# Kernel optimization log

Hardware: AMD Instinct MI355X
Metric: run time of the kernel (lower is better)

The kernel has to match this reference:

```python
import jax, jax.numpy as jnp
import numpy as np

B, S, D, E, H, K = 2, 2048, 1024, 8, 4096, 2


def setup_inputs() -> dict:
    key = jax.random.key(0)
    ks = jax.random.split(key, 8)
    w = lambda i, shape: jax.random.normal(ks[i], shape, jnp.float32) * 0.02
    return {
        "x": jax.random.normal(ks[0], (B, S, D), jnp.float32),
        "noise": jax.random.normal(ks[1], (B, S, E), jnp.float32),
        "Wg": w(2, (E, D)),
        "noise_weight": jnp.zeros((E,), jnp.float32),
        "W1": w(3, (E, D, H)),
        "b1": jnp.zeros((E, H), jnp.float32),
        "W2": w(4, (E, D, H)),
        "b2": jnp.zeros((E, H), jnp.float32),
        "Wp": w(5, (E, H, D)),
        "bp": jnp.zeros((E, D), jnp.float32),
        "k": K,
    }


def reference(x, noise, Wg, noise_weight, W1, b1, W2, b2, Wp, bp, k):
    Bb, Ss, Dd = x.shape
    Ee = Wg.shape[0]
    # --- noisy top-k gate (noisy_std = 1.0) ---
    logits = jnp.einsum('bsd,ed->bse', x, Wg)
    noisy = logits + noise * noise_weight            # [B,S,E]
    vals, idx = jax.lax.top_k(noisy, k)              # [B,S,k]
    oh = jax.nn.one_hot(idx, Ee, dtype=x.dtype)      # [B,S,k,E]
    sel = oh.sum(axis=-2) > 0                        # [B,S,E] selected mask
    scat = (oh * vals[..., None]).sum(axis=-2)       # scatter topk logits
    sparse = jnp.where(sel, scat, -jnp.inf)
    gate = jax.nn.softmax(sparse, axis=-1)           # zero weight off-topk
    # --- dense-equivalent expert compute (gate==0 off top-k => same math as masked dispatch) ---
    xf = x.reshape(Bb * Ss, Dd)                      # [T,D]
    gf = gate.reshape(Bb * Ss, Ee)                   # [T,E]
    h1 = jnp.einsum('td,edh->eth', xf, W1) + b1[:, None, :]
    h2 = jnp.einsum('td,edh->eth', xf, W2) + b2[:, None, :]
    hh = h1 * jax.nn.silu(h2)                        # SwiGLU
    outs = jnp.einsum('eth,ehd->etd', hh, Wp) + bp[:, None, :]
    final = jnp.einsum('etd,te->td', outs, gf).reshape(Bb, Ss, Dd)
    return final, idx
```

## Files before the change

kernel.cpp:

```cpp
#include <hip/hip_runtime.h>
#include <math.h>

#define Bc 2
#define Sc 2048
#define Dc 1024
#define Ec 8
#define Hc 4096
#define Tc (Bc*Sc)
#define NSLOT (Tc*2)
#define FINAL_N ((size_t)Tc*Dc)
#define BK 32

typedef float f32x4 __attribute__((ext_vector_type(4)));
typedef __bf16 bf16x8 __attribute__((ext_vector_type(8)));

__device__ __forceinline__ unsigned short f2bf(float f) {
    union { float f; unsigned int u; } v; v.f = f;
    return (unsigned short)((v.u + 0x7fffu + ((v.u >> 16) & 1u)) >> 16);
}

__device__ __forceinline__ void gload16(const unsigned short* g, unsigned short* l) {
    __builtin_amdgcn_global_load_lds(
        (const __attribute__((address_space(1))) unsigned int*)g,
        (__attribute__((address_space(3))) unsigned int*)l,
        16, 0, 0);
}

__global__ void k_cvt_x(const float* __restrict__ x, unsigned short* __restrict__ xbf) {
    int gid = blockIdx.x * 256 + threadIdx.x;
    const float4* p = (const float4*)x + (size_t)gid * 2;
    float4 a = p[0], b = p[1];
    ushort4 r0 = { f2bf(a.x), f2bf(a.y), f2bf(a.z), f2bf(a.w) };
    ushort4 r1 = { f2bf(b.x), f2bf(b.y), f2bf(b.z), f2bf(b.w) };
    ushort4* o = (ushort4*)xbf + (size_t)gid * 2;
    o[0] = r0; o[1] = r1;
}

__global__ void k_transpose_cvt2(const float* __restrict__ inA, const float* __restrict__ inB,
                                 unsigned short* __restrict__ outA, unsigned short* __restrict__ outB,
                                 int R, int C, int nz_per_mat) {
    __shared__ float tile[64][65];
    int z = blockIdx.z;
    const float* in; unsigned short* out;
    if (z < nz_per_mat) { in = inA; out = outA; }
    else { in = inB; out = outB; z -= nz_per_mat; }
    size_t base = (size_t)z * (size_t)R * C;
    int cb = blockIdx.x * 64, rb = blockIdx.y * 64;
    int t = threadIdx.x;
    int q = t & 15, g = t >> 4;
    #pragma unroll
    for (int j = 0; j < 4; j++) {
        int row = g + 16*j;
        float4 v = *(const float4*)&in[base + (size_t)(rb+row)*C + cb + q*4];
        tile[row][q*4+0] = v.x; tile[row][q*4+1] = v.y;
        tile[row][q*4+2] = v.z; tile[row][q*4+3] = v.w;
    }
    __syncthreads();
    #pragma unroll
    for (int j = 0; j < 4; j++) {
        int co = g + 16*j;
        ushort4 o;
        o.x = f2bf(tile[q*4+0][co]); o.y = f2bf(tile[q*4+1][co]);
        o.z = f2bf(tile[q*4+2][co]); o.w = f2bf(tile[q*4+3][co]);
        *(ushort4*)&out[base + (size_t)(cb+co)*R + rb + q*4] = o;
    }
}

__global__ void k_gate(const float* __restrict__ x, const float* __restrict__ noise,
                       const float* __restrict__ Wg, const float* __restrict__ nw,
                       float* __restrict__ out_idx, int* __restrict__ counts,
                       int* __restrict__ tok_top, float* __restrict__ tok_w) {
    int t = blockIdx.x;
    int lane = threadIdx.x;
    const float* xr = x + (size_t)t * Dc;
    double acc[Ec];
    #pragma unroll
    for (int e = 0; e < Ec; e++) acc[e] = 0.0;
    for (int i = 0; i < Dc/64; i++) {
        int d = lane + i*64;
        double xv = (double)xr[d];
        #pragma unroll
        for (int e = 0; e < Ec; e++) acc[e] += xv * (double)Wg[e*Dc + d];
    }
    #pragma unroll
    for (int e = 0; e < Ec; e++)
        for (int off = 32; off > 0; off >>= 1)
            acc[e] += __shfl_down(acc[e], off);
    if (lane == 0) {
        double noisy[Ec];
        #pragma unroll
        for (int e = 0; e < Ec; e++)
            noisy[e] = acc[e] + (double)noise[t*Ec + e] * (double)nw[e];
        int i0 = 0;
        for (int e = 1; e < Ec; e++) if (noisy[e] > noisy[i0]) i0 = e;
        int i1 = -1;
        for (int e = 0; e < Ec; e++) {
            if (e == i0) continue;
            if (i1 < 0 || noisy[e] > noisy[i1]) i1 = e;
        }
        double ee = exp(noisy[i1] - noisy[i0]);
        float w0 = (float)(1.0 / (1.0 + ee));
        float w1 = (float)(ee / (1.0 + ee));
        out_idx[t*2 + 0] = (float)i0;
        out_idx[t*2 + 1] = (float)i1;
        tok_top[t*2] = i0; tok_top[t*2+1] = i1;
        tok_w[t*2] = w0;   tok_w[t*2+1] = w1;
        atomicAdd(&counts[i0], 1);
        atomicAdd(&counts[i1], 1);
    }
}

__global__ void k_scan(const int* __restrict__ counts, int* __restrict__ offsets) {
    if (threadIdx.x == 0) {
        int s = 0;
        for (int e = 0; e < Ec; e++) { offsets[e] = s; s += counts[e]; }
        offsets[Ec] = s;
    }
}

__global__ void k_fill(const int* __restrict__ tok_top, const int* __restrict__ offsets,
                       int* __restrict__ fill, int* __restrict__ slot_token,
                       int* __restrict__ slot_of) {
    int t = blockIdx.x * 256 + threadIdx.x;
    if (t >= Tc) return;
    #pragma unroll
    for (int j = 0; j < 2; j++) {
        int e = tok_top[t*2 + j];
        int pos = atomicAdd(&fill[e], 1);
        int slot = offsets[e] + pos;
        slot_token[slot] = t;
        slot_of[t*2 + j] = slot;
    }
}

__global__ __launch_bounds__(256, 2) void k_gemm1(
    const unsigned short* __restrict__ xbf,
    const unsigned short* __restrict__ w1t, const unsigned short* __restrict__ w2t,
    const float* __restrict__ b1, const float* __restrict__ b2,
    const int* __restrict__ counts, const int* __restrict__ offsets,
    const int* __restrict__ slot_token,
    unsigned short* __restrict__ hh) {
    int e = blockIdx.z;
    int n_e = counts[e];
    int m0 = blockIdx.y * 128;
    if (m0 >= n_e) return;
    int base = offsets[e];
    int n0 = blockIdx.x * 128;

    __shared__ __align__(16) unsigned short lA0[128*BK],  lB10[128*BK], lB20[128*BK];
    __shared__ __align__(16) unsigned short lA1[128*BK],  lB11[128*BK], lB21[128*BK];
    __shared__ int tlist[128];

    int tid = threadIdx.x;
    if (tid < 128) {
        int r = m0 + tid; if (r > n_e - 1) r = n_e - 1;
        tlist[tid] = slot_token[base + r];
    }
    __syncthreads();

    int wid = tid >> 6, lane = tid & 63;
    int wr = wid >> 1, wc = wid & 1;

    int rl = lane >> 2, s = lane & 3;
    int r0 = wid*32 + rl, r1 = r0 + 16;
    int c0 = s ^ ((r0 >> 1) & 3);
    int c1 = s ^ ((r1 >> 1) & 3);
    int t0 = tlist[r0], t1 = tlist[r1];
    const size_t wbase = ((size_t)e * Hc + n0) * Dc;
    const unsigned short* pa0  = xbf + (size_t)t0*Dc + c0*8;
    const unsigned short* pa1  = xbf + (size_t)t1*Dc + c1*8;
    const unsigned short* pb10 = w1t + wbase + (size_t)r0*Dc + c0*8;
    const unsigned short* pb11 = w1t + wbase + (size_t)r1*Dc + c1*8;
    const unsigned short* pb20 = w2t + wbase + (size_t)r0*Dc + c0*8;
    const unsigned short* pb21 = w2t + wbase + (size_t)r1*Dc + c1*8;
    int wofs = wid*1024;

    f32x4 acc1[4][4], acc2[4][4];
    #pragma unroll
    for (int m = 0; m < 4; m++)
        #pragma unroll
        for (int n = 0; n < 4; n++)
            #pragma unroll
            for (int j = 0; j < 4; j++) { acc1[m][n][j] = 0.0f; acc2[m][n][j] = 0.0f; }

    int arow = lane & 15, cr = lane >> 4;

    auto STAGE = [&](unsigned short* dA, unsigned short* dB1, unsigned short* dB2, int kk) {
        gload16(pa0  + kk, dA  + wofs);  gload16(pa1  + kk, dA  + wofs + 512);
        gload16(pb10 + kk, dB1 + wofs);  gload16(pb11 + kk, dB1 + wofs + 512);
        gload16(pb20 + kk, dB2 + wofs);  gload16(pb21 + kk, dB2 + wofs + 512);
    };
    auto COMPUTE = [&](const unsigned short* lA, const unsigned short* lB1,
                       const unsigned short* lB2) {
        bf16x8 a[4], bb1[4], bb2[4];
        #pragma unroll
        for (int m = 0; m < 4; m++) {
            int rr = wr*64 + m*16 + arow;
            int cc = cr ^ ((rr >> 1) & 3);
            a[m] = *(const bf16x8*)&lA[rr*BK + cc*8];
        }
        #pragma unroll
        for (int n = 0; n < 4; n++) {
            int rr = wc*64 + n*16 + arow;
            int cc = cr ^ ((rr >> 1) & 3);
            bb1[n] = *(const bf16x8*)&lB1[rr*BK + cc*8];
            bb2[n] = *(const bf16x8*)&lB2[rr*BK + cc*8];
        }
        #pragma unroll
        for (int m = 0; m < 4; m++)
            #pragma unroll
            for (int n = 0; n < 4; n++) {
                acc1[m][n] = __builtin_amdgcn_mfma_f32_16x16x32_bf16(a[m], bb1[n], acc1[m][n], 0, 0, 0);
                acc2[m][n] = __builtin_amdgcn_mfma_f32_16x16x32_bf16(a[m], bb2[n], acc2[m][n], 0, 0, 0);
            }
    };

    STAGE(lA0, lB10, lB20, 0);
    __syncthreads();
    const int NT = Dc / BK;
    for (int t = 0; t < NT; t += 2) {
        STAGE(lA1, lB11, lB21, (t+1)*BK);
        COMPUTE(lA0, lB10, lB20);
        __syncthreads();
        if (t + 2 < NT) STAGE(lA0, lB10, lB20, (t+2)*BK);
        COMPUTE(lA1, lB11, lB21);
        __syncthreads();
    }

    int lrow = (lane >> 4) * 4, lcol = lane & 15;
    #pragma unroll
    for (int n = 0; n < 4; n++) {
        int hcol = n0 + wc*64 + n*16 + lcol;
        float bias1 = b1[e*Hc + hcol], bias2 = b2[e*Hc + hcol];
        #pragma unroll
        for (int m = 0; m < 4; m++) {
            int rb = m0 + wr*64 + m*16 + lrow;
            #pragma unroll
            for (int j = 0; j < 4; j++) {
                int r = rb + j;
                if (r < n_e) {
                    float h1v = acc1[m][n][j] + bias1;
                    float h2v = acc2[m][n][j] + bias2;
                    float hhv = h1v * (h2v / (1.0f + expf(-h2v)));
                    hh[(size_t)(base + r)*Hc + hcol] = f2bf(hhv);
                }
            }
        }
    }
}

__global__ __launch_bounds__(256, 2) void k_gemm2(
    const unsigned short* __restrict__ hh,
    const unsigned short* __restrict__ wpt,
    const float* __restrict__ bp,
    const int* __restrict__ counts, const int* __restrict__ offsets,
    float* __restrict__ outb) {
    int e = blockIdx.z;
    int n_e = counts[e];
    int m0 = blockIdx.y * 128;
    if (m0 >= n_e) return;
    int base = offsets[e];
    int n0 = blockIdx.x * 128;

    __shared__ __align__(16) unsigned short lA0[128*BK], lB0[128*BK];
    __shared__ __align__(16) unsigned short lA1[128*BK], lB1[128*BK];

    int tid = threadIdx.x;
    int wid = tid >> 6, lane = tid & 63;
    int wr = wid >> 1, wc = wid & 1;

    int rl = lane >> 2, s = lane & 3;
    int r0 = wid*32 + rl, r1 = r0 + 16;
    int c0 = s ^ ((r0 >> 1) & 3);
    int c1 = s ^ ((r1 >> 1) & 3);
    int ar0 = m0 + r0; if (ar0 > n_e - 1) ar0 = n_e - 1;
    int ar1 = m0 + r1; if (ar1 > n_e - 1) ar1 = n_e - 1;
    const size_t wb = ((size_t)e * Dc + n0) * Hc;
    const unsigned short* pa0 = hh  + (size_t)(base + ar0)*Hc + c0*8;
    const unsigned short* pa1 = hh  + (size_t)(base + ar1)*Hc + c1*8;
    const unsigned short* pb0 = wpt + wb + (size_t)r0*Hc + c0*8;
    const unsigned short* pb1 = wpt + wb + (size_t)r1*Hc + c1*8;
    int wofs = wid*1024;

    f32x4 acc[4][4];
    #pragma unroll
    for (int m = 0; m < 4; m++)
        #pragma unroll
        for (int n = 0; n < 4; n++)
            #pragma unroll
            for (int j = 0; j < 4; j++) acc[m][n][j] = 0.0f;

    int arow = lane & 15, cr = lane >> 4;

    auto STAGE = [&](unsigned short* dA, unsigned short* dB, int kk) {
        gload16(pa0 + kk, dA + wofs);  gload16(pa1 + kk, dA + wofs + 512);
        gload16(pb0 + kk, dB + wofs);  gload16(pb1 + kk, dB + wofs + 512);
    };
    auto COMPUTE = [&](const unsigned short* lA, const unsigned short* lB) {
        bf16x8 a[4], b[4];
        #pragma unroll
        for (int m = 0; m < 4; m++) {
            int rr = wr*64 + m*16 + arow;
            int cc = cr ^ ((rr >> 1) & 3);
            a[m] = *(const bf16x8*)&lA[rr*BK + cc*8];
        }
        #pragma unroll
        for (int n = 0; n < 4; n++) {
            int rr = wc*64 + n*16 + arow;
            int cc = cr ^ ((rr >> 1) & 3);
            b[n] = *(const bf16x8*)&lB[rr*BK + cc*8];
        }
        #pragma unroll
        for (int m = 0; m < 4; m++)
            #pragma unroll
            for (int n = 0; n < 4; n++)
                acc[m][n] = __builtin_amdgcn_mfma_f32_16x16x32_bf16(a[m], b[n], acc[m][n], 0, 0, 0);
    };

    STAGE(lA0, lB0, 0);
    __syncthreads();
    const int NT = Hc / BK;
    for (int t = 0; t < NT; t += 2) {
        STAGE(lA1, lB1, (t+1)*BK);
        COMPUTE(lA0, lB0);
        __syncthreads();
        if (t + 2 < NT) STAGE(lA0, lB0, (t+2)*BK);
        COMPUTE(lA1, lB1);
        __syncthreads();
    }

    int lrow = (lane >> 4) * 4, lcol = lane & 15;
    #pragma unroll
    for (int n = 0; n < 4; n++) {
        int dcol = n0 + wc*64 + n*16 + lcol;
        float bias = bp[e*Dc + dcol];
        #pragma unroll
        for (int m = 0; m < 4; m++) {
            int rb = m0 + wr*64 + m*16 + lrow;
            #pragma unroll
            for (int j = 0; j < 4; j++) {
                int r = rb + j;
                if (r < n_e)
                    outb[(size_t)(base + r)*Dc + dcol] = acc[m][n][j] + bias;
            }
        }
    }
}

__global__ void k_combine(const float* __restrict__ outb, const int* __restrict__ slot_of,
                          const float* __restrict__ tok_w, float* __restrict__ final_out) {
    int gid = blockIdx.x * 256 + threadIdx.x;
    int t = gid >> 8;
    int c = (gid & 255) * 4;
    int s0 = slot_of[t*2], s1 = slot_of[t*2 + 1];
    float w0 = tok_w[t*2], w1 = tok_w[t*2 + 1];
    float4 o0 = *(const float4*)&outb[(size_t)s0*Dc + c];
    float4 o1 = *(const float4*)&outb[(size_t)s1*Dc + c];
    float4 r;
    r.x = w0*o0.x + w1*o1.x;
    r.y = w0*o0.y + w1*o1.y;
    r.z = w0*o0.z + w1*o1.z;
    r.w = w0*o0.w + w1*o1.w;
    *(float4*)&final_out[(size_t)t*Dc + c] = r;
}

extern "C" void kernel_launch(void* const* d_in, const int* in_sizes, int n_in,
                              void* d_out, int out_size, void* d_ws, size_t ws_size,
                              hipStream_t stream) {
    (void)in_sizes; (void)n_in; (void)out_size; (void)ws_size;
    const float* x     = (const float*)d_in[0];
    const float* noise = (const float*)d_in[1];
    const float* Wg    = (const float*)d_in[2];
    const float* nw    = (const float*)d_in[3];
    const float* W1    = (const float*)d_in[4];
    const float* b1    = (const float*)d_in[5];
    const float* W2    = (const float*)d_in[6];
    const float* b2    = (const float*)d_in[7];
    const float* Wp    = (const float*)d_in[8];
    const float* bp    = (const float*)d_in[9];

    char* ws = (char*)d_ws;
    size_t off = 0;
    unsigned short* XBF = (unsigned short*)(ws + off); off += (size_t)Tc*Dc*2;
    unsigned short* W1T = (unsigned short*)(ws + off); off += (size_t)Ec*Dc*Hc*2;
    unsigned short* W2T = (unsigned short*)(ws + off); off += (size_t)Ec*Dc*Hc*2;
    unsigned short* WPT = (unsigned short*)(ws + off); off += (size_t)Ec*Hc*Dc*2;
    unsigned short* HH  = (unsigned short*)(ws + off); off += (size_t)NSLOT*Hc*2;
    float*          OUTB= (float*)(ws + off);          off += (size_t)NSLOT*Dc*4;
    int*   counts    = (int*)(ws + off);
    int*   fill      = (int*)(ws + off + 32);
    int*   offsets   = (int*)(ws + off + 64);
    int*   tok_top   = (int*)(ws + off + 128);
    float* tok_w     = (float*)(ws + off + 128 + (size_t)Tc*2*4);
    int*   slot_token= (int*)(ws + off + 128 + (size_t)Tc*2*8);
    int*   slot_of   = (int*)(ws + off + 128 + (size_t)Tc*2*8 + (size_t)NSLOT*4);

    float* final_out = (float*)d_out;
    float* idx_out   = (float*)d_out + FINAL_N;

    hipMemsetAsync(counts, 0, 64, stream);

    k_cvt_x<<<(Tc*Dc/8)/256, 256, 0, stream>>>(x, XBF);
    k_transpose_cvt2<<<dim3(Hc/64, Dc/64, 2*Ec), 256, 0, stream>>>(W1, W2, W1T, W2T, Dc, Hc, Ec);
    k_transpose_cvt2<<<dim3(Dc/64, Hc/64, Ec), 256, 0, stream>>>(Wp, Wp, WPT, WPT, Hc, Dc, Ec);

    k_gate<<<Tc, 64, 0, stream>>>(x, noise, Wg, nw, idx_out, counts, tok_top, tok_w);
    k_scan<<<1, 64, 0, stream>>>(counts, offsets);
    k_fill<<<Tc/256, 256, 0, stream>>>(tok_top, offsets, fill, slot_token, slot_of);

    k_gemm1<<<dim3(Hc/128, Tc/128, Ec), 256, 0, stream>>>(XBF, W1T, W2T, b1, b2,
                                                          counts, offsets, slot_token, HH);
    k_gemm2<<<dim3(Dc/128, Tc/128, Ec), 256, 0, stream>>>(HH, WPT, bp, counts, offsets, OUTB);
    k_combine<<<(Tc*Dc/4)/256, 256, 0, stream>>>(OUTB, slot_of, tok_w, final_out);
}
```

Before: 690.8 us.

## Enlarge expert GEMM tiles to 256x128 with 512 threads and triple-buffered pipeline

Both grouped expert GEMMs move to 256-row by 128-col tiles with 8 waves per block. The old double buffer with two syncthreads per step becomes a three-stage LDS ring, using explicit vmcnt/lgkmcnt waits, raw s_barrier fences and s_setprio around the MFMA bursts. gemm2 also loads a 64-wide K step per stage. The aim is to hide global-load latency and reuse more of each weight tile, at the cost of more LDS per block and hand-counted waitcnt values that must match the number of in-flight loads.

```diff
diff --git a/kernel.cpp b/kernel.cpp
--- a/kernel.cpp
+++ b/kernel.cpp
@@ -24,6 +24,12 @@
         (const __attribute__((address_space(1))) unsigned int*)g,
         (__attribute__((address_space(3))) unsigned int*)l,
         16, 0, 0);
+}
+
+__device__ __forceinline__ void fence_bar() {
+    __builtin_amdgcn_sched_barrier(0);
+    asm volatile("s_barrier" ::: "memory");
+    __builtin_amdgcn_sched_barrier(0);
 }
 
 __global__ void k_cvt_x(const float* __restrict__ x, unsigned short* __restrict__ xbf) {
@@ -133,7 +139,12 @@
     }
 }
 
-__global__ __launch_bounds__(256, 2) void k_gemm1(
+#define BM1 256
+#define BN1 128
+#define A1SZ (BM1*BK)
+#define W1SZ (BN1*BK)
+
+__global__ __launch_bounds__(512, 2) void k_gemm1(
     const unsigned short* __restrict__ xbf,
     const unsigned short* __restrict__ w1t, const unsigned short* __restrict__ w2t,
     const float* __restrict__ b1, const float* __restrict__ b2,
@@ -142,17 +153,18 @@
     unsigned short* __restrict__ hh) {
     int e = blockIdx.z;
     int n_e = counts[e];
-    int m0 = blockIdx.y * 128;
+    int m0 = blockIdx.y * BM1;
     if (m0 >= n_e) return;
     int base = offsets[e];
-    int n0 = blockIdx.x * 128;
-
-    __shared__ __align__(16) unsigned short lA0[128*BK],  lB10[128*BK], lB20[128*BK];
-    __shared__ __align__(16) unsigned short lA1[128*BK],  lB11[128*BK], lB21[128*BK];
-    __shared__ int tlist[128];
+    int n0 = blockIdx.x * BN1;
+
+    __shared__ __align__(16) unsigned short sA[3*A1SZ];
+    __shared__ __align__(16) unsigned short sW1[3*W1SZ];
+    __shared__ __align__(16) unsigned short sW2[3*W1SZ];
+    __shared__ int tlist[BM1];
 
     int tid = threadIdx.x;
-    if (tid < 128) {
+    if (tid < BM1) {
         int r = m0 + tid; if (r > n_e - 1) r = n_e - 1;
         tlist[tid] = slot_token[base + r];
     }
@@ -161,19 +173,19 @@
     int wid = tid >> 6, lane = tid & 63;
     int wr = wid >> 1, wc = wid & 1;
 
-    int rl = lane >> 2, s = lane & 3;
-    int r0 = wid*32 + rl, r1 = r0 + 16;
-    int c0 = s ^ ((r0 >> 1) & 3);
-    int c1 = s ^ ((r1 >> 1) & 3);
-    int t0 = tlist[r0], t1 = tlist[r1];
-    const size_t wbase = ((size_t)e * Hc + n0) * Dc;
-    const unsigned short* pa0  = xbf + (size_t)t0*Dc + c0*8;
-    const unsigned short* pa1  = xbf + (size_t)t1*Dc + c1*8;
-    const unsigned short* pb10 = w1t + wbase + (size_t)r0*Dc + c0*8;
-    const unsigned short* pb11 = w1t + wbase + (size_t)r1*Dc + c1*8;
-    const unsigned short* pb20 = w2t + wbase + (size_t)r0*Dc + c0*8;
-    const unsigned short* pb21 = w2t + wbase + (size_t)r1*Dc + c1*8;
-    int wofs = wid*1024;
+    int rl = lane >> 2, sc_ = lane & 3;
+    int rA0 = wid*32 + rl, rA1 = rA0 + 16;
+    int rB  = wid*16 + rl;
+    int cA0 = sc_ ^ ((rA0 >> 1) & 3);
+    int cA1 = sc_ ^ ((rA1 >> 1) & 3);
+    int cB  = sc_ ^ ((rB  >> 1) & 3);
+    int tA0 = tlist[rA0], tA1 = tlist[rA1];
+    const unsigned short* pa0 = xbf + (size_t)tA0*Dc + cA0*8;
+    const unsigned short* pa1 = xbf + (size_t)tA1*Dc + cA1*8;
+    const size_t wb = ((size_t)e * Hc + n0) * Dc;
+    const unsigned short* pw1 = w1t + wb + (size_t)rB*Dc + cB*8;
+    const unsigned short* pw2 = w2t + wb + (size_t)rB*Dc + cB*8;
+    int aofs = wid*1024, bofs = wid*512;
 
     f32x4 acc1[4][4], acc2[4][4];
     #pragma unroll
@@ -185,46 +197,70 @@
 
     int arow = lane & 15, cr = lane >> 4;
 
-    auto STAGE = [&](unsigned short* dA, unsigned short* dB1, unsigned short* dB2, int kk) {
-        gload16(pa0  + kk, dA  + wofs);  gload16(pa1  + kk, dA  + wofs + 512);
-        gload16(pb10 + kk, dB1 + wofs);  gload16(pb11 + kk, dB1 + wofs + 512);
-        gload16(pb20 + kk, dB2 + wofs);  gload16(pb21 + kk, dB2 + wofs + 512);
+    auto STAGE_A = [&](int buf, int kk) {
+        unsigned short* d = sA + buf*A1SZ + aofs;
+        gload16(pa0 + kk, d);
+        gload16(pa1 + kk, d + 512);
     };
-    auto COMPUTE = [&](const unsigned short* lA, const unsigned short* lB1,
-                       const unsigned short* lB2) {
-        bf16x8 a[4], bb1[4], bb2[4];
+    auto STAGE_W = [&](int buf, int kk) {
+        gload16(pw1 + kk, sW1 + buf*W1SZ + bofs);
+        gload16(pw2 + kk, sW2 + buf*W1SZ + bofs);
+    };
+
+    STAGE_A(0, 0);  STAGE_W(0, 0);
+    STAGE_A(1, BK); STAGE_W(1, BK);
+
+    const int NT = Dc / BK;
+    int ib = 0;
+    for (int t = 0; t < NT; ++t) {
+        int is = ib + 2; if (is >= 3) is -= 3;
+        if (t + 2 < NT) {
+            STAGE_A(is, (t+2)*BK);
+            asm volatile("s_waitcnt vmcnt(6)" ::: "memory");
+        } else if (t + 1 < NT) {
+            asm volatile("s_waitcnt vmcnt(4)" ::: "memory");
+        } else {
+            asm volatile("s_waitcnt vmcnt(0)" ::: "memory");
+        }
+        fence_bar();
+        const unsigned short* lA = sA  + ib*A1SZ;
+        const unsigned short* l1 = sW1 + ib*W1SZ;
+        const unsigned short* l2 = sW2 + ib*W1SZ;
+        bf16x8 af[4], w1f[4], w2f[4];
         #pragma unroll
         for (int m = 0; m < 4; m++) {
             int rr = wr*64 + m*16 + arow;
             int cc = cr ^ ((rr >> 1) & 3);
-            a[m] = *(const bf16x8*)&lA[rr*BK + cc*8];
+            af[m] = *(const bf16x8*)&lA[rr*BK + cc*8];
         }
         #pragma unroll
         for (int n = 0; n < 4; n++) {
             int rr = wc*64 + n*16 + arow;
             int cc = cr ^ ((rr >> 1) & 3);
-            bb1[n] = *(const bf16x8*)&lB1[rr*BK + cc*8];
-            bb2[n] = *(const bf16x8*)&lB2[rr*BK + cc*8];
-        }
+            w1f[n] = *(const bf16x8*)&l1[rr*BK + cc*8];
+        }
+        if (t + 2 < NT) STAGE_W(is, (t+2)*BK);
+        asm volatile("s_waitcnt lgkmcnt(0)" ::: "memory");
+        fence_bar();
+        __builtin_amdgcn_s_setprio(1);
         #pragma unroll
         for (int m = 0; m < 4; m++)
             #pragma unroll
-            for (int n = 0; n < 4; n++) {
-                acc1[m][n] = __builtin_amdgcn_mfma_f32_16x16x32_bf16(a[m], bb1[n], acc1[m][n], 0, 0, 0);
-                acc2[m][n] = __builtin_amdgcn_mfma_f32_16x16x32_bf16(a[m], bb2[n], acc2[m][n], 0, 0, 0);
-            }
-    };
-
-    STAGE(lA0, lB10, lB20, 0);
-    __syncthreads();
-    const int NT = Dc / BK;
-    for (int t = 0; t < NT; t += 2) {
-        STAGE(lA1, lB11, lB21, (t+1)*BK);
-        COMPUTE(lA0, lB10, lB20);
-        __syncthreads();
-        if (t + 2 < NT) STAGE(lA0, lB10, lB20, (t+2)*BK);
-        COMPUTE(lA1, lB11, lB21);
-        __syncthreads();
+            for (int n = 0; n < 4; n++)
+                acc1[m][n] = __builtin_amdgcn_mfma_f32_16x16x32_bf16(af[m], w1f[n], acc1[m][n], 0, 0, 0);
+        #pragma unroll
+        for (int n = 0; n < 4; n++) {
+            int rr = wc*64 + n*16 + arow;
+            int cc = cr ^ ((rr >> 1) & 3);
+            w2f[n] = *(const bf16x8*)&l2[rr*BK + cc*8];
+        }
+        #pragma unroll
+        for (int m = 0; m < 4; m++)
+            #pragma unroll
+            for (int n = 0; n < 4; n++)
+                acc2[m][n] = __builtin_amdgcn_mfma_f32_16x16x32_bf16(af[m], w2f[n], acc2[m][n], 0, 0, 0);
+        __builtin_amdgcn_s_setprio(0);
+        ib = ib + 1; if (ib == 3) ib = 0;
     }
 
     int lrow = (lane >> 4) * 4, lcol = lane & 15;
@@ -249,7 +285,12 @@
     }
 }
 
-__global__ __launch_bounds__(256, 2) void k_gemm2(
+#define BM2 256
+#define BN2 128
+#define A2SZ (BM2*BK)
+#define B2SZ (BN2*BK)
+
+__global__ __launch_bounds__(512, 2) void k_gemm2(
     const unsigned short* __restrict__ hh,
     const unsigned short* __restrict__ wpt,
     const float* __restrict__ bp,
@@ -257,30 +298,30 @@
     float* __restrict__ outb) {
     int e = blockIdx.z;
     int n_e = counts[e];
-    int m0 = blockIdx.y * 128;
+    int m0 = blockIdx.y * BM2;
     if (m0 >= n_e) return;
     int base = offsets[e];
-    int n0 = blockIdx.x * 128;
-
-    __shared__ __align__(16) unsigned short lA0[128*BK], lB0[128*BK];
-    __shared__ __align__(16) unsigned short lA1[128*BK], lB1[128*BK];
+    int n0 = blockIdx.x * BN2;
+
+    __shared__ __align__(16) unsigned short sA[3*2*A2SZ];
+    __shared__ __align__(16) unsigned short sB[3*2*B2SZ];
 
     int tid = threadIdx.x;
     int wid = tid >> 6, lane = tid & 63;
     int wr = wid >> 1, wc = wid & 1;
 
-    int rl = lane >> 2, s = lane & 3;
-    int r0 = wid*32 + rl, r1 = r0 + 16;
-    int c0 = s ^ ((r0 >> 1) & 3);
-    int c1 = s ^ ((r1 >> 1) & 3);
-    int ar0 = m0 + r0; if (ar0 > n_e - 1) ar0 = n_e - 1;
-    int ar1 = m0 + r1; if (ar1 > n_e - 1) ar1 = n_e - 1;
-    const size_t wb = ((size_t)e * Dc + n0) * Hc;
-    const unsigned short* pa0 = hh  + (size_t)(base + ar0)*Hc + c0*8;
-    const unsigned short* pa1 = hh  + (size_t)(base + ar1)*Hc + c1*8;
-    const unsigned short* pb0 = wpt + wb + (size_t)r0*Hc + c0*8;
-    const unsigned short* pb1 = wpt + wb + (size_t)r1*Hc + c1*8;
-    int wofs = wid*1024;
+    int rl = lane >> 2, sc_ = lane & 3;
+    int rA0 = wid*32 + rl, rA1 = rA0 + 16;
+    int rB  = wid*16 + rl;
+    int cA0 = sc_ ^ ((rA0 >> 1) & 3);
+    int cA1 = sc_ ^ ((rA1 >> 1) & 3);
+    int cB  = sc_ ^ ((rB  >> 1) & 3);
+    int gr0 = m0 + rA0; if (gr0 > n_e - 1) gr0 = n_e - 1;
+    int gr1 = m0 + rA1; if (gr1 > n_e - 1) gr1 = n_e - 1;
+    const unsigned short* pa0 = hh + (size_t)(base + gr0)*Hc + cA0*8;
+    const unsigned short* pa1 = hh + (size_t)(base + gr1)*Hc + cA1*8;
+    const unsigned short* pb  = wpt + ((size_t)e*Dc + n0 + rB)*Hc + cB*8;
+    int aofs = wid*1024, bofs = wid*512;
 
     f32x4 acc[4][4];
     #pragma unroll
@@ -292,41 +333,73 @@
 
     int arow = lane & 15, cr = lane >> 4;
 
-    auto STAGE = [&](unsigned short* dA, unsigned short* dB, int kk) {
-        gload16(pa0 + kk, dA + wofs);  gload16(pa1 + kk, dA + wofs + 512);
-        gload16(pb0 + kk, dB + wofs);  gload16(pb1 + kk, dB + wofs + 512);
+    auto STAGE_A = [&](int buf, int kk) {
+        unsigned short* d = sA + buf*(2*A2SZ) + aofs;
+        gload16(pa0 + kk, d);            gload16(pa1 + kk, d + 512);
+        gload16(pa0 + kk + BK, d + A2SZ); gload16(pa1 + kk + BK, d + A2SZ + 512);
     };
-    auto COMPUTE = [&](const unsigned short* lA, const unsigned short* lB) {
-        bf16x8 a[4], b[4];
+    auto STAGE_B = [&](int buf, int kk) {
+        unsigned short* d = sB + buf*(2*B2SZ) + bofs;
+        gload16(pb + kk, d);
+        gload16(pb + kk + BK, d + B2SZ);
+    };
+
+    STAGE_A(0, 0);  STAGE_B(0, 0);
+    STAGE_A(1, 64); STAGE_B(1, 64);
+
+    const int NT = Hc / 64;
+    int ib = 0;
+    for (int t = 0; t < NT; ++t) {
+        int is = ib + 2; if (is >= 3) is -= 3;
+        if (t + 2 < NT) {
+            STAGE_A(is, (t+2)*64);
+            asm volatile("s_waitcnt vmcnt(10)" ::: "memory");
+        } else if (t + 1 < NT) {
+            asm volatile("s_waitcnt vmcnt(6)" ::: "memory");
+        } else {
+            asm volatile("s_waitcnt vmcnt(0)" ::: "memory");
+        }
+        fence_bar();
+        const unsigned short* lA0 = sA + ib*(2*A2SZ);
+        const unsigned short* lA1 = lA0 + A2SZ;
+        const unsigned short* lB0 = sB + ib*(2*B2SZ);
+        const unsigned short* lB1 = lB0 + B2SZ;
+        bf16x8 af[2][4], wf[2][4];
         #pragma unroll
         for (int m = 0; m < 4; m++) {
             int rr = wr*64 + m*16 + arow;
             int cc = cr ^ ((rr >> 1) & 3);
-            a[m] = *(const bf16x8*)&lA[rr*BK + cc*8];
+            af[0][m] = *(const bf16x8*)&lA0[rr*BK + cc*8];
+            af[1][m] = *(const bf16x8*)&lA1[rr*BK + cc*8];
         }
         #pragma unroll
         for (int n = 0; n < 4; n++) {
             int rr = wc*64 + n*16 + arow;
             int cc = cr ^ ((rr >> 1) & 3);
-            b[n] = *(const bf16x8*)&lB[rr*BK + cc*8];
-        }
+            wf[0][n] = *(const bf16x8*)&lB0[rr*BK + cc*8];
+        }
+        if (t + 2 < NT) STAGE_B(is, (t+2)*64);
+        asm volatile("s_waitcnt lgkmcnt(0)" ::: "memory");
+        fence_bar();
+        __builtin_amdgcn_s_setprio(1);
         #pragma unroll
         for (int m = 0; m < 4; m++)
             #pragma unroll
             for (int n = 0; n < 4; n++)
-                acc[m][n] = __builtin_amdgcn_mfma_f32_16x16x32_bf16(a[m], b[n], acc[m][n], 0, 0, 0);
-    };
-
-    STAGE(lA0, lB0, 0);
-    __syncthreads();
-    const int NT = Hc / BK;
-    for (int t = 0; t < NT; t += 2) {
-        STAGE(lA1, lB1, (t+1)*BK);
-        COMPUTE(lA0, lB0);
-        __syncthreads();
-        if (t + 2 < NT) STAGE(lA0, lB0, (t+2)*BK);
-        COMPUTE(lA1, lB1);
-        __syncthreads();
+                acc[m][n] = __builtin_amdgcn_mfma_f32_16x16x32_bf16(af[0][m], wf[0][n], acc[m][n], 0, 0, 0);
+        #pragma unroll
+        for (int n = 0; n < 4; n++) {
+            int rr = wc*64 + n*16 + arow;
+            int cc = cr ^ ((rr >> 1) & 3);
+            wf[1][n] = *(const bf16x8*)&lB1[rr*BK + cc*8];
+        }
+        #pragma unroll
+        for (int m = 0; m < 4; m++)
+            #pragma unroll
+            for (int n = 0; n < 4; n++)
+                acc[m][n] = __builtin_amdgcn_mfma_f32_16x16x32_bf16(af[1][m], wf[1][n], acc[m][n], 0, 0, 0);
+        __builtin_amdgcn_s_setprio(0);
+        ib = ib + 1; if (ib == 3) ib = 0;
     }
 
     int lrow = (lane >> 4) * 4, lcol = lane & 15;
@@ -408,8 +481,8 @@
     k_scan<<<1, 64, 0, stream>>>(counts, offsets);
     k_fill<<<Tc/256, 256, 0, stream>>>(tok_top, offsets, fill, slot_token, slot_of);
 
-    k_gemm1<<<dim3(Hc/128, Tc/128, Ec), 256, 0, stream>>>(XBF, W1T, W2T, b1, b2,
+    k_gemm1<<<dim3(Hc/BN1, Tc/BM1, Ec), 512, 0, stream>>>(XBF, W1T, W2T, b1, b2,
                                                           counts, offsets, slot_token, HH);
-    k_gemm2<<<dim3(Dc/128, Tc/128, Ec), 256, 0, stream>>>(HH, WPT, bp, counts, offsets, OUTB);
+    k_gemm2<<<dim3(Dc/BN2, Tc/BM2, Ec), 512, 0, stream>>>(HH, WPT, bp, counts, offsets, OUTB);
     k_combine<<<(Tc*Dc/4)/256, 256, 0, stream>>>(OUTB, slot_of, tok_w, final_out);
 }
```

After: 682.7 us. No clear change (-1.2%).
